# Kernel optimization log

Measured on AMD Instinct MI355X. Metric: run time of the kernel, lower is better.

The kernel has to match this reference:

```python
import jax, jax.numpy as jnp
import numpy as np

HIDDEN = 1024
NUM_HEADS = 16
HEAD_DIM = HIDDEN // NUM_HEADS
ROPE_BASE = 10000.0
LN_EPS = 1e-8


def _rope_cos_sin(seq_len, dim, dtype=jnp.float32):
    inv_freq = 1.0 / (ROPE_BASE ** (jnp.arange(0, dim, 2, dtype=jnp.float32) / dim))
    t = jnp.arange(seq_len, dtype=jnp.float32)
    freqs = jnp.einsum('i,j->ij', t, inv_freq)          # [S, dim/2]
    emb = jnp.concatenate([freqs, freqs], axis=-1)       # [S, dim]
    return jnp.cos(emb).astype(dtype), jnp.sin(emb).astype(dtype)


def _rotate_half(x):
    x1, x2 = jnp.split(x, 2, axis=-1)
    return jnp.concatenate([-x2, x1], axis=-1)


def setup_inputs() -> dict:
    key = jax.random.key(0)
    ks = jax.random.split(key, 8)
    B, S, H = 4, 2048, HIDDEN
    x = jax.random.normal(ks[0], (B, S, H), dtype=jnp.float32)
    # causal mask, True = attend
    attn_mask = jnp.tril(jnp.ones((S, S), dtype=bool))[None].repeat(B, axis=0)
    lim_p = 1.0 / np.sqrt(H)
    Wp = jax.random.uniform(ks[1], (H, 4 * H), minval=-lim_p, maxval=lim_p, dtype=jnp.float32)
    bp = jax.random.uniform(ks[2], (4 * H,), minval=-lim_p, maxval=lim_p, dtype=jnp.float32)
    ln_g = jnp.ones((H,), dtype=jnp.float32)
    ln_b = jnp.zeros((H,), dtype=jnp.float32)
    Wt = jax.random.uniform(ks[3], (H, H), minval=-lim_p, maxval=lim_p, dtype=jnp.float32)
    bt = jax.random.uniform(ks[4], (H,), minval=-lim_p, maxval=lim_p, dtype=jnp.float32)
    return {"x": x, "attn_mask": attn_mask, "Wp": Wp, "bp": bp,
            "ln_g": ln_g, "ln_b": ln_b, "Wt": Wt, "bt": bt}


def reference(x, attn_mask, Wp, bp, ln_g, ln_b, Wt, bt):
    B, S, H = x.shape
    nh, hd = NUM_HEADS, HEAD_DIM
    proj = x @ Wp + bp                                   # [B,S,4H]
    U, V, Q, K = jnp.split(proj, 4, axis=-1)
    # [B, nh, S, hd]
    Q = Q.reshape(B, S, nh, hd).transpose(0, 2, 1, 3)
    K = K.reshape(B, S, nh, hd).transpose(0, 2, 1, 3)
    V = V.reshape(B, S, nh, hd).transpose(0, 2, 1, 3)
    cos, sin = _rope_cos_sin(S, hd, x.dtype)             # [S, hd]
    Qr = Q * cos + _rotate_half(Q) * sin
    Kr = K * cos + _rotate_half(K) * sin
    scale = hd ** -0.5
    scores = jnp.einsum('bhqd,bhkd->bhqk', Qr, Kr) * scale
    # masked positions -> sigmoid(-inf) == 0; use where for grad safety
    attn = jnp.where(attn_mask[:, None, :, :], jax.nn.sigmoid(scores), 0.0)
    attn_out = jnp.einsum('bhqk,bhkd->bhqd', attn, V)
    attn_out = attn_out.transpose(0, 2, 1, 3).reshape(B, S, H)
    mu = jnp.mean(attn_out, axis=-1, keepdims=True)
    var = jnp.var(attn_out, axis=-1, keepdims=True)
    attn_out = (attn_out - mu) / jnp.sqrt(var + LN_EPS) * ln_g + ln_b
    gated = jax.nn.silu(U) * attn_out
    out = gated @ Wt + bt
    return x + out
```

## Files before the change

### kernel.cpp

```cpp
#include <hip/hip_runtime.h>
#include <math.h>

#define H 1024
#define NH 16
#define HD 64
#define B_ 4
#define S_ 2048
#define ROWS (B_*S_)

#define QSCALE (-0.1803368801111664f)
#define ROPE_C (9.210340371976184f / 32.0f)

typedef __bf16 bf16x2_t __attribute__((ext_vector_type(2)));
typedef __bf16 bf16x4_t __attribute__((ext_vector_type(4)));
typedef __bf16 bf16x8_t __attribute__((ext_vector_type(8)));
typedef float floatx4_t __attribute__((ext_vector_type(4)));
typedef float floatx16_t __attribute__((ext_vector_type(16)));

#define GLOAD_LDS16(gp, lp)                                                        \
    __builtin_amdgcn_global_load_lds(                                              \
        (const __attribute__((address_space(1))) unsigned int*)(gp),               \
        (__attribute__((address_space(3))) unsigned int*)(lp), 16, 0, 0)

__global__ __launch_bounds__(256)
void prep_kernel(const float* __restrict__ x, const float* __restrict__ Wp,
                 const float* __restrict__ Wt,
                 __bf16* __restrict__ Ax, __bf16* __restrict__ Wp_t,
                 __bf16* __restrict__ Wt_t)
{
    __shared__ __bf16 t[32][33];
    const int flat = blockIdx.x;
    const int tid = threadIdx.x;

    if (flat < 8192) {
        size_t i = (size_t)flat * 256 + tid;
        float4 v = *reinterpret_cast<const float4*>(&x[i * 4]);
        bf16x4_t w = { (__bf16)v.x, (__bf16)v.y, (__bf16)v.z, (__bf16)v.w };
        *reinterpret_cast<bf16x4_t*>(&Ax[i * 4]) = w;
        return;
    }
    const float* W; __bf16* Wo; int K, N, bn, bk;
    if (flat < 12288) {
        int id = flat - 8192;  W = Wp; Wo = Wp_t; K = 1024; N = 4096;
        bn = (id & 127) * 32;  bk = (id >> 7) * 32;
    } else {
        int id = flat - 12288; W = Wt; Wo = Wt_t; K = 1024; N = 1024;
        bn = (id & 31) * 32;   bk = (id >> 5) * 32;
    }
    const int tx = tid & 31, ty = tid >> 5;
#pragma unroll
    for (int i = 0; i < 4; i++) {
        int r = ty + i * 8;
        t[tx][r] = (__bf16)W[(size_t)(bk + r) * N + bn + tx];
    }
    __syncthreads();
#pragma unroll
    for (int i = 0; i < 4; i++) {
        int r = ty + i * 8;
        Wo[(size_t)(bn + r) * K + bk + tx] = t[r][tx];
    }
}


__global__ __launch_bounds__(256)
void gemm_out(const __bf16* __restrict__ A, const __bf16* __restrict__ Bt,
              const float* __restrict__ bias, const float* __restrict__ resid,
              float* __restrict__ C, int M, int N, int K)
{
    __shared__ __bf16 As[128 * 32];
    __shared__ __bf16 Bs[128 * 32];

    const int tid  = threadIdx.x;
    const int wave = tid >> 6, lane = tid & 63;
    const int l31 = lane & 31, half = lane >> 5;
    const int wm = wave & 1, wn = wave >> 1;
    const int m0 = blockIdx.y * 128, n0 = blockIdx.x * 128;

    const int srow = lane >> 2;
    const int skc  = (((lane & 3) ^ ((srow >> 1) & 3)) * 8);

    const int fsw = (l31 >> 1) & 3;
    int aoff[2][2], boff[2][2];
#pragma unroll
    for (int mt = 0; mt < 2; mt++)
#pragma unroll
        for (int ks = 0; ks < 2; ks++) {
            int ra = wm * 64 + mt * 32 + l31;
            int rb = wn * 64 + mt * 32 + l31;
            int c = ks * 2 + half;
            aoff[mt][ks] = ra * 32 + ((c ^ fsw) * 8);
            boff[mt][ks] = rb * 32 + ((c ^ fsw) * 8);
        }

    floatx16_t acc[2][2];
#pragma unroll
    for (int i = 0; i < 2; i++)
#pragma unroll
        for (int j = 0; j < 2; j++) acc[i][j] = (floatx16_t)(0.f);

    for (int k0 = 0; k0 < K; k0 += 32) {
#pragma unroll
        for (int p = 0; p < 2; p++) {
            int i = wave * 2 + p;
            int rl = i * 16 + srow;
            GLOAD_LDS16(A  + (size_t)(m0 + rl) * K + k0 + skc, &As[i * 512]);
            GLOAD_LDS16(Bt + (size_t)(n0 + rl) * K + k0 + skc, &Bs[i * 512]);
        }
        __syncthreads();

        bf16x8_t af[2][2], bf[2][2];
#pragma unroll
        for (int mt = 0; mt < 2; mt++)
#pragma unroll
            for (int ks = 0; ks < 2; ks++) {
                af[mt][ks] = *reinterpret_cast<const bf16x8_t*>(&As[aoff[mt][ks]]);
                bf[mt][ks] = *reinterpret_cast<const bf16x8_t*>(&Bs[boff[mt][ks]]);
            }
#pragma unroll
        for (int ks = 0; ks < 2; ks++)
#pragma unroll
            for (int mt = 0; mt < 2; mt++)
#pragma unroll
                for (int nt = 0; nt < 2; nt++)
                    acc[mt][nt] = __builtin_amdgcn_mfma_f32_32x32x16_bf16(
                        af[mt][ks], bf[nt][ks], acc[mt][nt], 0, 0, 0);
        __syncthreads();
    }

#pragma unroll
    for (int mt = 0; mt < 2; mt++) {
#pragma unroll
        for (int nt = 0; nt < 2; nt++) {
            int col = n0 + wn * 64 + nt * 32 + l31;
            float bv = bias[col];
#pragma unroll
            for (int reg = 0; reg < 16; reg++) {
                int rowf = (reg & 3) + 8 * (reg >> 2) + 4 * half;
                int row = m0 + wm * 64 + mt * 32 + rowf;
                C[(size_t)row * N + col] = acc[mt][nt][reg] + bv + resid[(size_t)row * N + col];
            }
        }
    }
}

__global__ __launch_bounds__(256)
void gemm_proj(const __bf16* __restrict__ A, const __bf16* __restrict__ Bt,
               const float* __restrict__ bias,
               __bf16* __restrict__ Ug, __bf16* __restrict__ Vh,
               __bf16* __restrict__ Qh, __bf16* __restrict__ Kh)
{
    const int K = 1024;
    __shared__ __bf16 As[128 * 32];
    __shared__ __bf16 Bs[128 * 32];

    const int tid  = threadIdx.x;
    const int wave = tid >> 6, lane = tid & 63;
    const int l31 = lane & 31, half = lane >> 5;
    const int wm = wave & 1, wn = wave >> 1;
    const int m0 = blockIdx.y * 128, n0 = blockIdx.x * 128;

    const int srow = lane >> 2;
    const int skc  = (((lane & 3) ^ ((srow >> 1) & 3)) * 8);

    const int fsw = (l31 >> 1) & 3;
    int aoff[2][2], boff[2][2];
#pragma unroll
    for (int mt = 0; mt < 2; mt++)
#pragma unroll
        for (int ks = 0; ks < 2; ks++) {
            int ra = wm * 64 + mt * 32 + l31;
            int rb = wn * 64 + mt * 32 + l31;
            int c = ks * 2 + half;
            aoff[mt][ks] = ra * 32 + ((c ^ fsw) * 8);
            boff[mt][ks] = rb * 32 + ((c ^ fsw) * 8);
        }

    floatx16_t acc[2][2];
#pragma unroll
    for (int i = 0; i < 2; i++)
#pragma unroll
        for (int j = 0; j < 2; j++) acc[i][j] = (floatx16_t)(0.f);

    for (int k0 = 0; k0 < K; k0 += 32) {
#pragma unroll
        for (int p = 0; p < 2; p++) {
            int i = wave * 2 + p;
            int rl = i * 16 + srow;
            GLOAD_LDS16(A  + (size_t)(m0 + rl) * K + k0 + skc, &As[i * 512]);
            GLOAD_LDS16(Bt + (size_t)(n0 + rl) * K + k0 + skc, &Bs[i * 512]);
        }
        __syncthreads();

        bf16x8_t af[2][2], bf[2][2];
#pragma unroll
        for (int mt = 0; mt < 2; mt++)
#pragma unroll
            for (int ks = 0; ks < 2; ks++) {
                af[mt][ks] = *reinterpret_cast<const bf16x8_t*>(&As[aoff[mt][ks]]);
                bf[mt][ks] = *reinterpret_cast<const bf16x8_t*>(&Bs[boff[mt][ks]]);
            }
#pragma unroll
        for (int ks = 0; ks < 2; ks++)
#pragma unroll
            for (int mt = 0; mt < 2; mt++)
#pragma unroll
                for (int nt = 0; nt < 2; nt++)
                    acc[mt][nt] = __builtin_amdgcn_mfma_f32_32x32x16_bf16(
                        af[mt][ks], bf[nt][ks], acc[mt][nt], 0, 0, 0);
        __syncthreads();
    }

    float bv[2];
    bv[0] = bias[n0 + wn * 64 + l31];
    bv[1] = bias[n0 + wn * 64 + 32 + l31];

    if (n0 < 1024) {
#pragma unroll
        for (int mt = 0; mt < 2; mt++)
#pragma unroll
            for (int nt = 0; nt < 2; nt++) {
                int col = n0 + wn * 64 + nt * 32 + l31;
#pragma unroll
                for (int reg = 0; reg < 16; reg++) {
                    int rowf = (reg & 3) + 8 * (reg >> 2) + 4 * half;
                    int row = m0 + wm * 64 + mt * 32 + rowf;
                    Ug[(size_t)row * 1024 + col] = (__bf16)(acc[mt][nt][reg] + bv[nt]);
                }
            }
    } else if (n0 < 2048) {
        const int h = ((n0 - 1024) >> 6) + wn;
#pragma unroll
        for (int mt = 0; mt < 2; mt++)
#pragma unroll
            for (int reg = 0; reg < 16; reg++) {
                int rowf = (reg & 3) + 8 * (reg >> 2) + 4 * half;
                int row = m0 + wm * 64 + mt * 32 + rowf;
                int b = row >> 11, s = row & (S_ - 1);
                size_t orow = ((size_t)(b * NH + h) * S_ + s) * 64;
                Vh[orow + l31]      = (__bf16)(acc[mt][0][reg] + bv[0]);
                Vh[orow + 32 + l31] = (__bf16)(acc[mt][1][reg] + bv[1]);
            }
    } else {
        const bool isQ = (n0 < 3072);
        const int h = ((n0 - (isQ ? 2048 : 3072)) >> 6) + wn;
        __bf16* dst = isQ ? Qh : Kh;
        const float sc = isQ ? QSCALE : 1.0f;
        const float inv = __expf(-(float)l31 * ROPE_C);
#pragma unroll
        for (int mt = 0; mt < 2; mt++)
#pragma unroll
            for (int reg = 0; reg < 16; reg++) {
                int rowf = (reg & 3) + 8 * (reg >> 2) + 4 * half;
                int row = m0 + wm * 64 + mt * 32 + rowf;
                int b = row >> 11, s = row & (S_ - 1);
                size_t orow = ((size_t)(b * NH + h) * S_ + s) * 64;
                float sn, cs;
                __sincosf((float)s * inv, &sn, &cs);
                float lo = acc[mt][0][reg] + bv[0];
                float hi = acc[mt][1][reg] + bv[1];
                dst[orow + l31]      = (__bf16)((lo * cs - hi * sn) * sc);
                dst[orow + 32 + l31] = (__bf16)((hi * cs + lo * sn) * sc);
            }
    }
}

__global__ __launch_bounds__(256)
void transpose_v(const __bf16* __restrict__ Vh, __bf16* __restrict__ VtG)
{
    const int tid = threadIdx.x;
    const int st = blockIdx.x, bh = blockIdx.y;
    const int s0 = st * 64;
    const int d = tid & 63, k16 = tid >> 6;
    __bf16 vals[16];
#pragma unroll
    for (int j = 0; j < 16; j++) {
        int k = s0 + k16 * 16 + j;
        vals[j] = Vh[((size_t)bh * S_ + k) * 64 + d];
    }
    size_t orow = ((size_t)(bh * 64 + d)) * S_ + s0 + k16 * 16;
    *reinterpret_cast<bf16x8_t*>(&VtG[orow])     = *reinterpret_cast<bf16x8_t*>(&vals[0]);
    *reinterpret_cast<bf16x8_t*>(&VtG[orow + 8]) = *reinterpret_cast<bf16x8_t*>(&vals[8]);
}

__global__ __launch_bounds__(256)
void attn_mfma(const __bf16* __restrict__ Qh, const __bf16* __restrict__ Kh,
               const __bf16* __restrict__ VtG, __bf16* __restrict__ attn_out)
{
    __shared__ __bf16 Ks[2][4096];
    __shared__ __bf16 Vt[2][4096];
    __shared__ __bf16 Ps[4][16][72];

    const int tid = threadIdx.x, wave = tid >> 6, lane = tid & 63;
    const int quad = lane >> 4, ln = lane & 15;
    const int qt = (S_ / 128 - 1) - (blockIdx.x >> 6);
    const int hb = blockIdx.x & 63, h = hb & 15, b = hb >> 4, bh = b * NH + h;
    const int Q0 = qt * 128, T0 = 2 * qt;
    const int wl = wave * 16 + ln;

    const size_t qr = ((size_t)bh * S_ + Q0 + wl) * 64;
    bf16x8_t qa[2][2];
    qa[0][0] = *reinterpret_cast<const bf16x8_t*>(&Qh[qr + quad * 8]);
    qa[0][1] = *reinterpret_cast<const bf16x8_t*>(&Qh[qr + 32 + quad * 8]);
    qa[1][0] = *reinterpret_cast<const bf16x8_t*>(&Qh[qr + 4096 + quad * 8]);
    qa[1][1] = *reinterpret_cast<const bf16x8_t*>(&Qh[qr + 4096 + 32 + quad * 8]);

    const int sr = lane >> 3, scl = (lane & 7) ^ sr;
    const int c0 = wave * 2, c1 = c0 + 1;
    const size_t khead = (size_t)bh * S_ * 64;
    const int koff0 = (c0 * 8 + sr) * 64 + scl * 8;
    const int koff1 = (c1 * 8 + sr) * 64 + scl * 8;
    const size_t vg0 = ((size_t)bh * 64 + c0 * 8 + sr) * S_ + scl * 8;
    const size_t vg1 = ((size_t)bh * 64 + c1 * 8 + sr) * S_ + scl * 8;

    const int m7 = ln & 7;
    int ka[4][2];
#pragma unroll
    for (int nt = 0; nt < 4; nt++) {
        int row = nt * 16 + ln;
        ka[nt][0] = row * 64 + ((quad ^ m7) << 3);
        ka[nt][1] = row * 64 + (((quad + 4) ^ m7) << 3);
    }

    floatx4_t o[2][4];
#pragma unroll
    for (int s = 0; s < 2; s++)
#pragma unroll
        for (int dt = 0; dt < 4; dt++) o[s][dt] = (floatx4_t){0.f, 0.f, 0.f, 0.f};

    GLOAD_LDS16(Kh  + khead + koff0, &Ks[0][c0 * 512]);
    GLOAD_LDS16(Kh  + khead + koff1, &Ks[0][c1 * 512]);
    GLOAD_LDS16(VtG + vg0,           &Vt[0][c0 * 512]);
    GLOAD_LDS16(VtG + vg1,           &Vt[0][c1 * 512]);

    for (int kt = 0; kt <= T0 + 1; kt++) {
        const int buf = kt & 1;
        __syncthreads();
        if (kt <= T0) {
            const int nb = buf ^ 1;
            const size_t kg = khead + (size_t)(kt + 1) * 4096;
            GLOAD_LDS16(Kh  + kg + koff0,            &Ks[nb][c0 * 512]);
            GLOAD_LDS16(Kh  + kg + koff1,            &Ks[nb][c1 * 512]);
            GLOAD_LDS16(VtG + vg0 + (kt + 1) * 64,   &Vt[nb][c0 * 512]);
            GLOAD_LDS16(VtG + vg1 + (kt + 1) * 64,   &Vt[nb][c1 * 512]);
        }

        bf16x8_t kf[4][2], vf[4][2];
#pragma unroll
        for (int nt = 0; nt < 4; nt++) {
            kf[nt][0] = *reinterpret_cast<const bf16x8_t*>(&Ks[buf][ka[nt][0]]);
            kf[nt][1] = *reinterpret_cast<const bf16x8_t*>(&Ks[buf][ka[nt][1]]);
        }
#pragma unroll
        for (int dt = 0; dt < 4; dt++) {
            vf[dt][0] = *reinterpret_cast<const bf16x8_t*>(&Vt[buf][ka[dt][0]]);
            vf[dt][1] = *reinterpret_cast<const bf16x8_t*>(&Vt[buf][ka[dt][1]]);
        }

        const int mode0 = (kt < T0) ? 0 : ((kt == T0) ? 1 : 2);
        const int mode1 = (kt <= T0) ? 0 : 1;

#pragma unroll
        for (int s = 0; s < 2; s++) {
            const int mode = s ? mode1 : mode0;
            if (mode == 2) continue;

            floatx4_t st[4];
#pragma unroll
            for (int nt = 0; nt < 4; nt++) {
                floatx4_t acc = (floatx4_t){0.f, 0.f, 0.f, 0.f};
                acc = __builtin_amdgcn_mfma_f32_16x16x32_bf16(kf[nt][0], qa[s][0], acc, 0, 0, 0);
                acc = __builtin_amdgcn_mfma_f32_16x16x32_bf16(kf[nt][1], qa[s][1], acc, 0, 0, 0);
                st[nt] = acc;
            }

#pragma unroll
            for (int nt = 0; nt < 4; nt++) {
                bf16x4_t pk;
#pragma unroll
                for (int r = 0; r < 4; r++) {
                    float a = st[nt][r];
                    if (mode == 1) {
                        int kl = nt * 16 + quad * 4 + r;
                        a = (kl <= wl) ? a : __builtin_inff();
                    }
                    float p = __builtin_amdgcn_rcpf(1.f + __builtin_amdgcn_exp2f(a));
                    pk[r] = (__bf16)p;
                }
                *reinterpret_cast<bf16x4_t*>(&Ps[wave][ln][nt * 16 + quad * 4]) = pk;
            }

            const __bf16* prow = &Ps[wave][ln][quad * 8];
            bf16x8_t p0 = *reinterpret_cast<const bf16x8_t*>(prow);
            bf16x8_t p1 = *reinterpret_cast<const bf16x8_t*>(prow + 32);
#pragma unroll
            for (int dt = 0; dt < 4; dt++) {
                o[s][dt] = __builtin_amdgcn_mfma_f32_16x16x32_bf16(p0, vf[dt][0], o[s][dt], 0, 0, 0);
                o[s][dt] = __builtin_amdgcn_mfma_f32_16x16x32_bf16(p1, vf[dt][1], o[s][dt], 0, 0, 0);
            }
        }
    }

#pragma unroll
    for (int s = 0; s < 2; s++) {
        const int qrow_g = b * S_ + Q0 + s * 64 + wave * 16 + quad * 4;
#pragma unroll
        for (int dt = 0; dt < 4; dt++) {
#pragma unroll
            for (int reg = 0; reg < 4; reg++) {
                attn_out[(size_t)(qrow_g + reg) * H + h * 64 + dt * 16 + ln] =
                    (__bf16)o[s][dt][reg];
            }
        }
    }
}

__global__ __launch_bounds__(256)
void ln_gate_kernel(const __bf16* __restrict__ attn_out, const __bf16* __restrict__ Ug,
                    const float* __restrict__ ln_g, const float* __restrict__ ln_b,
                    __bf16* __restrict__ gated)
{
    const int row = blockIdx.x;
    const int tid = threadIdx.x;

    bf16x4_t vb = *reinterpret_cast<const bf16x4_t*>(&attn_out[(size_t)row * H + tid * 4]);
    float v0 = (float)vb[0], v1 = (float)vb[1], v2 = (float)vb[2], v3 = (float)vb[3];
    float s  = v0 + v1 + v2 + v3;
    float sq = v0 * v0 + v1 * v1 + v2 * v2 + v3 * v3;
#pragma unroll
    for (int off = 32; off > 0; off >>= 1) {
        s  += __shfl_down(s, off);
        sq += __shfl_down(sq, off);
    }
    __shared__ float ps[4], pq[4];
    int wave = tid >> 6, lane = tid & 63;
    if (lane == 0) { ps[wave] = s; pq[wave] = sq; }
    __syncthreads();
    float ts = ps[0] + ps[1] + ps[2] + ps[3];
    float tq = pq[0] + pq[1] + pq[2] + pq[3];
    float mu  = ts * (1.f / (float)H);
    float var = tq * (1.f / (float)H) - mu * mu;
    float rstd = rsqrtf(var + 1e-8f);

    bf16x4_t ub = *reinterpret_cast<const bf16x4_t*>(&Ug[(size_t)row * 1024 + tid * 4]);
    float4 g  = *reinterpret_cast<const float4*>(&ln_g[tid * 4]);
    float4 bb = *reinterpret_cast<const float4*>(&ln_b[tid * 4]);
    float u0 = (float)ub[0], u1 = (float)ub[1], u2 = (float)ub[2], u3 = (float)ub[3];
    bf16x4_t outv;
    outv[0] = (__bf16)(((v0 - mu) * rstd * g.x + bb.x) * (u0 / (1.f + __expf(-u0))));
    outv[1] = (__bf16)(((v1 - mu) * rstd * g.y + bb.y) * (u1 / (1.f + __expf(-u1))));
    outv[2] = (__bf16)(((v2 - mu) * rstd * g.z + bb.z) * (u2 / (1.f + __expf(-u2))));
    outv[3] = (__bf16)(((v3 - mu) * rstd * g.w + bb.w) * (u3 / (1.f + __expf(-u3))));
    *reinterpret_cast<bf16x4_t*>(&gated[(size_t)row * H + tid * 4]) = outv;
}

extern "C" void kernel_launch(void* const* d_in, const int* in_sizes, int n_in,
                              void* d_out, int out_size, void* d_ws, size_t ws_size,
                              hipStream_t stream)
{
    const float* x    = (const float*)d_in[0];
    const float* Wp   = (const float*)d_in[2];
    const float* bp   = (const float*)d_in[3];
    const float* ln_g = (const float*)d_in[4];
    const float* ln_b = (const float*)d_in[5];
    const float* Wt   = (const float*)d_in[6];
    const float* bt   = (const float*)d_in[7];
    float* out = (float*)d_out;

    char* ws = (char*)d_ws;
    const size_t MB = 1024 * 1024;
    __bf16* Ug    = (__bf16*)(ws);
    __bf16* Vh    = (__bf16*)(ws + 16  * MB);
    __bf16* Qh    = (__bf16*)(ws + 32  * MB);
    __bf16* Kh    = (__bf16*)(ws + 48  * MB);
    __bf16* attn  = (__bf16*)(ws + 64  * MB);
    __bf16* gated = (__bf16*)(ws + 80  * MB);
    __bf16* VtG   = (__bf16*)(ws + 96  * MB);
    __bf16* Ax    = (__bf16*)(ws + 112 * MB);
    __bf16* Wp_t  = (__bf16*)(ws + 128 * MB);
    __bf16* Wt_t  = (__bf16*)(ws + 136 * MB);

    prep_kernel<<<13312, 256, 0, stream>>>(x, Wp, Wt, Ax, Wp_t, Wt_t);

    dim3 g1(4096 / 128, ROWS / 128);
    gemm_proj<<<g1, 256, 0, stream>>>(Ax, Wp_t, bp, Ug, Vh, Qh, Kh);

    transpose_v<<<dim3(S_ / 64, B_ * NH), 256, 0, stream>>>(Vh, VtG);

    attn_mfma<<<(S_ / 128) * NH * B_, 256, 0, stream>>>(Qh, Kh, VtG, attn);

    ln_gate_kernel<<<ROWS, 256, 0, stream>>>(attn, Ug, ln_g, ln_b, gated);

    dim3 g3(1024 / 128, ROWS / 128);
    gemm_out<<<g3, 256, 0, stream>>>(gated, Wt_t, bt, x, out, ROWS, 1024, 1024);
}
```

Measured before the change: 344.2 us.

## Rewrite projection GEMM with 256x256 tiles and multi-stage pipelined LDS loads

The projection GEMM moves from 128x128 tiles with a single LDS buffer to 256x256 tiles, 512 threads, 16x16x32 MFMAs and a double-buffered, 128KB LDS pipeline. Global-to-LDS loads for later k-tiles are interleaved with compute phases and separated by explicit barriers and vmcnt waits. It also adds s_setprio around the MFMA blocks. The aim is more data reuse per tile and hiding global load latency behind matrix math. The cost is heavy register and LDS use, which limits occupancy, and fewer blocks in the grid.

```diff
diff --git a/kernel.cpp b/kernel.cpp
--- a/kernel.cpp
+++ b/kernel.cpp
@@ -62,6 +62,162 @@
 }
 
 
+#define MIN15(x) ((x) < 15 ? (x) : 15)
+
+#define STAGE_A(buf, h, tile) do { int _kb = (tile) * 64 + (h) * 32;               \
+        char* _lb = lwA + ((buf) * 2 + (h)) * 16384;                               \
+        GLOAD_LDS16(a_src0 + _kb, _lb);                                            \
+        GLOAD_LDS16(a_src1 + _kb, _lb + 1024); } while (0)
+#define STAGE_B(buf, h, tile) do { int _kb = (tile) * 64 + (h) * 32;               \
+        char* _lb = lwB + ((buf) * 2 + (h)) * 16384;                               \
+        GLOAD_LDS16(b_src0 + _kb, _lb);                                            \
+        GLOAD_LDS16(b_src1 + _kb, _lb + 1024); } while (0)
+
+__global__ __launch_bounds__(512, 2)
+void gemm_proj(const __bf16* __restrict__ A, const __bf16* __restrict__ Bt,
+               const float* __restrict__ bias,
+               __bf16* __restrict__ Ug, __bf16* __restrict__ Vh,
+               __bf16* __restrict__ Qh, __bf16* __restrict__ Kh)
+{
+    __shared__ __attribute__((aligned(16))) char smem[131072];
+
+    const int tid  = threadIdx.x;
+    const int wave = tid >> 6, lane = tid & 63;
+    const int ln15 = lane & 15, q4 = lane >> 4;
+    const int wm = wave & 1, wn = wave >> 1;
+    const int m0 = blockIdx.y * 256, n0 = blockIdx.x * 256;
+
+    const int srow0 = wave * 32 + (lane >> 2);
+    const int csrc  = (lane & 3) ^ ((lane >> 3) & 3);
+    const __bf16* a_src0 = A  + (size_t)(m0 + srow0) * 1024 + csrc * 8;
+    const __bf16* a_src1 = a_src0 + (size_t)16 * 1024;
+    const __bf16* b_src0 = Bt + (size_t)(n0 + srow0) * 1024 + csrc * 8;
+    const __bf16* b_src1 = b_src0 + (size_t)16 * 1024;
+    char* lwA = smem + wave * 2048;
+    char* lwB = smem + 65536 + wave * 2048;
+
+    const int sl = (ln15 >> 1) & 3;
+    const int a_lane = (wm * 128 + ln15) * 64 + ((q4 ^ sl) << 4);
+    const int b_lane = (wn * 64  + ln15) * 64 + ((q4 ^ sl) << 4);
+
+    floatx4_t acc[8][4];
+#pragma unroll
+    for (int i = 0; i < 8; i++)
+#pragma unroll
+        for (int j = 0; j < 4; j++) acc[i][j] = (floatx4_t){0.f, 0.f, 0.f, 0.f};
+
+    STAGE_B(0, 0, 0); STAGE_A(0, 0, 0); STAGE_B(0, 1, 0); STAGE_A(0, 1, 0);
+    STAGE_B(1, 0, 1); STAGE_A(1, 0, 1); STAGE_B(1, 1, 1);
+    asm volatile("s_waitcnt vmcnt(6)" ::: "memory");
+    __builtin_amdgcn_s_barrier();
+
+    bf16x8_t bfr[4];
+
+    for (int it = 0; it < 8; ++it) {
+        const int T = 2 * it;
+#pragma unroll
+        for (int p = 0; p < 8; ++p) {
+            const int buf = p >> 2, sub = p & 3, mh = sub & 1, kk = sub >> 1;
+            const char* asl = smem + (buf * 2 + kk) * 16384;
+            const char* bsl = smem + 65536 + (buf * 2 + kk) * 16384;
+
+            if ((sub & 1) == 0) {
+#pragma unroll
+                for (int nf = 0; nf < 4; nf++)
+                    bfr[nf] = *reinterpret_cast<const bf16x8_t*>(bsl + b_lane + nf * 1024);
+            }
+            bf16x8_t af[4];
+#pragma unroll
+            for (int mfi = 0; mfi < 4; mfi++)
+                af[mfi] = *reinterpret_cast<const bf16x8_t*>(asl + a_lane + (mh * 4 + mfi) * 1024);
+
+            if      (p == 0) STAGE_A(1, 1, MIN15(T + 1));
+            else if (p == 1) STAGE_B(0, 0, MIN15(T + 2));
+            else if (p == 2) STAGE_A(0, 0, MIN15(T + 2));
+            else if (p == 3) STAGE_B(0, 1, MIN15(T + 2));
+            else if (p == 4) STAGE_A(0, 1, MIN15(T + 2));
+            else if (p == 5) STAGE_B(1, 0, MIN15(T + 3));
+            else if (p == 6) STAGE_A(1, 0, MIN15(T + 3));
+            else             STAGE_B(1, 1, MIN15(T + 3));
+
+            if (p == 3 || p == 7)
+                asm volatile("s_waitcnt vmcnt(6)" ::: "memory");
+            __builtin_amdgcn_s_barrier();
+
+            __builtin_amdgcn_s_setprio(1);
+#pragma unroll
+            for (int nf = 0; nf < 4; nf++)
+#pragma unroll
+                for (int mfi = 0; mfi < 4; mfi++)
+                    acc[mh * 4 + mfi][nf] = __builtin_amdgcn_mfma_f32_16x16x32_bf16(
+                        af[mfi], bfr[nf], acc[mh * 4 + mfi][nf], 0, 0, 0);
+            __builtin_amdgcn_s_setprio(0);
+            __builtin_amdgcn_s_barrier();
+        }
+    }
+    asm volatile("s_waitcnt vmcnt(0)" ::: "memory");
+
+    const int colbase = n0 + wn * 64;
+    float bv[4];
+#pragma unroll
+    for (int nf = 0; nf < 4; nf++) bv[nf] = bias[colbase + nf * 16 + ln15];
+
+    const int rowb = m0 + wm * 128 + q4 * 4;
+
+    if (n0 < 1024) {
+#pragma unroll
+        for (int mf = 0; mf < 8; mf++)
+#pragma unroll
+            for (int nf = 0; nf < 4; nf++) {
+                int col = colbase + nf * 16 + ln15;
+#pragma unroll
+                for (int reg = 0; reg < 4; reg++) {
+                    int row = rowb + mf * 16 + reg;
+                    Ug[(size_t)row * 1024 + col] = (__bf16)(acc[mf][nf][reg] + bv[nf]);
+                }
+            }
+    } else if (n0 < 2048) {
+        const int h = ((n0 - 1024) >> 6) + wn;
+#pragma unroll
+        for (int mf = 0; mf < 8; mf++)
+#pragma unroll
+            for (int reg = 0; reg < 4; reg++) {
+                int row = rowb + mf * 16 + reg;
+                int b = row >> 11, s = row & (S_ - 1);
+                size_t orow = ((size_t)(b * NH + h) * S_ + s) * 64;
+#pragma unroll
+                for (int nf = 0; nf < 4; nf++)
+                    Vh[orow + nf * 16 + ln15] = (__bf16)(acc[mf][nf][reg] + bv[nf]);
+            }
+    } else {
+        const bool isQ = (n0 < 3072);
+        const int h = ((n0 - (isQ ? 2048 : 3072)) >> 6) + wn;
+        __bf16* dst = isQ ? Qh : Kh;
+        const float sc = isQ ? QSCALE : 1.0f;
+        float inv[2];
+        inv[0] = __expf(-(float)(ln15)      * ROPE_C);
+        inv[1] = __expf(-(float)(16 + ln15) * ROPE_C);
+#pragma unroll
+        for (int mf = 0; mf < 8; mf++)
+#pragma unroll
+            for (int reg = 0; reg < 4; reg++) {
+                int row = rowb + mf * 16 + reg;
+                int b = row >> 11, s = row & (S_ - 1);
+                size_t orow = ((size_t)(b * NH + h) * S_ + s) * 64;
+#pragma unroll
+                for (int nf = 0; nf < 2; nf++) {
+                    float sn, cs;
+                    __sincosf((float)s * inv[nf], &sn, &cs);
+                    float lo = acc[mf][nf][reg]     + bv[nf];
+                    float hi = acc[mf][nf + 2][reg] + bv[nf + 2];
+                    int d = nf * 16 + ln15;
+                    dst[orow + d]      = (__bf16)((lo * cs - hi * sn) * sc);
+                    dst[orow + 32 + d] = (__bf16)((hi * cs + lo * sn) * sc);
+                }
+            }
+    }
+}
+
 __global__ __launch_bounds__(256)
 void gemm_out(const __bf16* __restrict__ A, const __bf16* __restrict__ Bt,
               const float* __restrict__ bias, const float* __restrict__ resid,
@@ -140,127 +296,6 @@
                 C[(size_t)row * N + col] = acc[mt][nt][reg] + bv + resid[(size_t)row * N + col];
             }
         }
-    }
-}
-
-__global__ __launch_bounds__(256)
-void gemm_proj(const __bf16* __restrict__ A, const __bf16* __restrict__ Bt,
-               const float* __restrict__ bias,
-               __bf16* __restrict__ Ug, __bf16* __restrict__ Vh,
-               __bf16* __restrict__ Qh, __bf16* __restrict__ Kh)
-{
-    const int K = 1024;
-    __shared__ __bf16 As[128 * 32];
-    __shared__ __bf16 Bs[128 * 32];
-
-    const int tid  = threadIdx.x;
-    const int wave = tid >> 6, lane = tid & 63;
-    const int l31 = lane & 31, half = lane >> 5;
-    const int wm = wave & 1, wn = wave >> 1;
-    const int m0 = blockIdx.y * 128, n0 = blockIdx.x * 128;
-
-    const int srow = lane >> 2;
-    const int skc  = (((lane & 3) ^ ((srow >> 1) & 3)) * 8);
-
-    const int fsw = (l31 >> 1) & 3;
-    int aoff[2][2], boff[2][2];
-#pragma unroll
-    for (int mt = 0; mt < 2; mt++)
-#pragma unroll
-        for (int ks = 0; ks < 2; ks++) {
-            int ra = wm * 64 + mt * 32 + l31;
-            int rb = wn * 64 + mt * 32 + l31;
-            int c = ks * 2 + half;
-            aoff[mt][ks] = ra * 32 + ((c ^ fsw) * 8);
-            boff[mt][ks] = rb * 32 + ((c ^ fsw) * 8);
-        }
-
-    floatx16_t acc[2][2];
-#pragma unroll
-    for (int i = 0; i < 2; i++)
-#pragma unroll
-        for (int j = 0; j < 2; j++) acc[i][j] = (floatx16_t)(0.f);
-
-    for (int k0 = 0; k0 < K; k0 += 32) {
-#pragma unroll
-        for (int p = 0; p < 2; p++) {
-            int i = wave * 2 + p;
-            int rl = i * 16 + srow;
-            GLOAD_LDS16(A  + (size_t)(m0 + rl) * K + k0 + skc, &As[i * 512]);
-            GLOAD_LDS16(Bt + (size_t)(n0 + rl) * K + k0 + skc, &Bs[i * 512]);
-        }
-        __syncthreads();
-
-        bf16x8_t af[2][2], bf[2][2];
-#pragma unroll
-        for (int mt = 0; mt < 2; mt++)
-#pragma unroll
-            for (int ks = 0; ks < 2; ks++) {
-                af[mt][ks] = *reinterpret_cast<const bf16x8_t*>(&As[aoff[mt][ks]]);
-                bf[mt][ks] = *reinterpret_cast<const bf16x8_t*>(&Bs[boff[mt][ks]]);
-            }
-#pragma unroll
-        for (int ks = 0; ks < 2; ks++)
-#pragma unroll
-            for (int mt = 0; mt < 2; mt++)
-#pragma unroll
-                for (int nt = 0; nt < 2; nt++)
-                    acc[mt][nt] = __builtin_amdgcn_mfma_f32_32x32x16_bf16(
-                        af[mt][ks], bf[nt][ks], acc[mt][nt], 0, 0, 0);
-        __syncthreads();
-    }
-
-    float bv[2];
-    bv[0] = bias[n0 + wn * 64 + l31];
-    bv[1] = bias[n0 + wn * 64 + 32 + l31];
-
-    if (n0 < 1024) {
-#pragma unroll
-        for (int mt = 0; mt < 2; mt++)
-#pragma unroll
-            for (int nt = 0; nt < 2; nt++) {
-                int col = n0 + wn * 64 + nt * 32 + l31;
-#pragma unroll
-                for (int reg = 0; reg < 16; reg++) {
-                    int rowf = (reg & 3) + 8 * (reg >> 2) + 4 * half;
-                    int row = m0 + wm * 64 + mt * 32 + rowf;
-                    Ug[(size_t)row * 1024 + col] = (__bf16)(acc[mt][nt][reg] + bv[nt]);
-                }
-            }
-    } else if (n0 < 2048) {
-        const int h = ((n0 - 1024) >> 6) + wn;
-#pragma unroll
-        for (int mt = 0; mt < 2; mt++)
-#pragma unroll
-            for (int reg = 0; reg < 16; reg++) {
-                int rowf = (reg & 3) + 8 * (reg >> 2) + 4 * half;
-                int row = m0 + wm * 64 + mt * 32 + rowf;
-                int b = row >> 11, s = row & (S_ - 1);
-                size_t orow = ((size_t)(b * NH + h) * S_ + s) * 64;
-                Vh[orow + l31]      = (__bf16)(acc[mt][0][reg] + bv[0]);
-                Vh[orow + 32 + l31] = (__bf16)(acc[mt][1][reg] + bv[1]);
-            }
-    } else {
-        const bool isQ = (n0 < 3072);
-        const int h = ((n0 - (isQ ? 2048 : 3072)) >> 6) + wn;
-        __bf16* dst = isQ ? Qh : Kh;
-        const float sc = isQ ? QSCALE : 1.0f;
-        const float inv = __expf(-(float)l31 * ROPE_C);
-#pragma unroll
-        for (int mt = 0; mt < 2; mt++)
-#pragma unroll
-            for (int reg = 0; reg < 16; reg++) {
-                int rowf = (reg & 3) + 8 * (reg >> 2) + 4 * half;
-                int row = m0 + wm * 64 + mt * 32 + rowf;
-                int b = row >> 11, s = row & (S_ - 1);
-                size_t orow = ((size_t)(b * NH + h) * S_ + s) * 64;
-                float sn, cs;
-                __sincosf((float)s * inv, &sn, &cs);
-                float lo = acc[mt][0][reg] + bv[0];
-                float hi = acc[mt][1][reg] + bv[1];
-                dst[orow + l31]      = (__bf16)((lo * cs - hi * sn) * sc);
-                dst[orow + 32 + l31] = (__bf16)((hi * cs + lo * sn) * sc);
-            }
     }
 }
 
@@ -481,8 +516,8 @@
 
     prep_kernel<<<13312, 256, 0, stream>>>(x, Wp, Wt, Ax, Wp_t, Wt_t);
 
-    dim3 g1(4096 / 128, ROWS / 128);
-    gemm_proj<<<g1, 256, 0, stream>>>(Ax, Wp_t, bp, Ug, Vh, Qh, Kh);
+    dim3 g1(4096 / 256, ROWS / 256);
+    gemm_proj<<<g1, 512, 0, stream>>>(Ax, Wp_t, bp, Ug, Vh, Qh, Kh);
 
     transpose_v<<<dim3(S_ / 64, B_ * NH), 256, 0, stream>>>(Vh, VtG);
 
```

Result: no change. 341.0 us (-0.9%).
